# Kernel tuning notes

Measured on AMD Instinct MI355X. Metric: run time of the kernel, lower is better.

Reference implementation:

```python
import jax, jax.numpy as jnp
import numpy as np

N = 100000   # nodes
E = 3200000  # edges (avg degree 32)
K = 3        # num_stacks
L = 4        # num_layers (ARMA iterations)
H = 16       # hidden channels
C = 1        # num_classes
BN_EPS = 1e-5


def setup_inputs() -> dict:
    key = jax.random.key(0)
    ks = jax.random.split(key, 16)
    s = 0.1  # weight scale
    return {
        "x": jax.random.normal(ks[0], (N, 1), dtype=jnp.float32),
        "edge_index": jax.random.randint(ks[1], (2, E), 0, N, dtype=jnp.int64),
        "edge_attr": jax.random.uniform(ks[2], (E,), dtype=jnp.float32),
        "batch": jnp.zeros((N,), dtype=jnp.int64),
        # ARMAConv 1: 1 -> 16, shared weights
        "w1_init": s * jax.random.normal(ks[3], (K, 1, H), dtype=jnp.float32),
        "w1": s * jax.random.normal(ks[4], (K, H, H), dtype=jnp.float32),
        "w1_root": s * jax.random.normal(ks[5], (K, 1, H), dtype=jnp.float32),
        "b1": s * jax.random.normal(ks[6], (K, 1, H), dtype=jnp.float32),
        "bn1_g": jnp.ones((H,), dtype=jnp.float32),
        "bn1_b": jnp.zeros((H,), dtype=jnp.float32),
        # ARMAConv 2: 16 -> 1, shared weights, act=None
        "w2_init": s * jax.random.normal(ks[7], (K, H, C), dtype=jnp.float32),
        "w2": s * jax.random.normal(ks[8], (K, C, C), dtype=jnp.float32),
        "w2_root": s * jax.random.normal(ks[9], (K, H, C), dtype=jnp.float32),
        "b2": s * jax.random.normal(ks[10], (K, 1, C), dtype=jnp.float32),
    }


def _arma_conv(x, row, col, norm, w_init, w, w_root, b, n_layers, use_relu):
    """PyG ARMAConv with shared_weights=True, eval-mode dropout (identity).
    x: [N,Fin]; returns mean over K stacks: [N,Fout]."""
    n = x.shape[0]
    root = jnp.einsum('nf,kfo->kno', x, w_root)      # [K,N,Fout]
    out = jnp.einsum('nf,kfo->kno', x, w_init)       # [K,N,Fout]
    for t in range(n_layers):
        if t > 0:
            out = jnp.einsum('kno,kop->knp', out, w)
        # message: gather at source, scale by norm; aggregate (scatter-add) at target
        m = (out[:, row, :] * norm[None, :, None]).transpose(1, 0, 2)  # [E,K,F]
        out = jax.ops.segment_sum(m, col, num_segments=n).transpose(1, 0, 2)
        out = out + root + b
        if use_relu:
            out = jax.nn.relu(out)
    return out.mean(axis=0)


def reference(x, edge_index, edge_attr, batch, w1_init, w1, w1_root, b1,
              bn1_g, bn1_b, w2_init, w2, w2_root, b2):
    row, col = edge_index[0], edge_index[1]
    n = x.shape[0]
    # gcn_norm without self-loops: D^{-1/2} A D^{-1/2}
    deg = jax.ops.segment_sum(edge_attr, col, num_segments=n)
    dinv = jnp.where(deg > 0, jax.lax.rsqrt(jnp.maximum(deg, 1e-12)), 0.0)
    norm = dinv[row] * edge_attr * dinv[col]

    h = _arma_conv(x, row, col, norm, w1_init, w1, w1_root, b1, L, True)
    # BatchNorm1d (batch statistics) + ReLU; dropout is identity in eval
    mu = h.mean(axis=0)
    var = h.var(axis=0)
    h = (h - mu) * jax.lax.rsqrt(var + BN_EPS) * bn1_g + bn1_b
    h = jax.nn.relu(h)

    h = _arma_conv(h, row, col, norm, w2_init, w2, w2_root, b2, L, False)
    return jax.nn.sigmoid(h)
```

## Files before the change

### kernel.cpp

```cpp
#include <hip/hip_runtime.h>
#include <math.h>

#define N_NODES 100000
#define N_EDGES 3200000
#define KH 48
#define FDIM 64
#define NH 16
#define BN_EPS 1e-5f
#define NBUCK 196
#define BSHIFT 9
#define BMASK 511
#define EPB 16384
#define NBLK1 196
#define CAP 18432
#define FIX 16777216.0f

typedef unsigned long long u64;
typedef unsigned int u32;
typedef unsigned short u16;

__device__ __forceinline__ u16 f2bf(float f) {
  u32 b = __float_as_uint(f);
  b += 0x7FFFu + ((b >> 16) & 1u);
  return (u16)(b >> 16);
}
__device__ __forceinline__ float bf2f(u32 s) {
  return __uint_as_float(s << 16);
}
__device__ __forceinline__ u32 rfl(u32 v) {
  return (u32)__builtin_amdgcn_readfirstlane((int)v);
}

__global__ __launch_bounds__(1024) void bucket_scatter_kernel(
    const int* __restrict__ row, const int* __restrict__ col,
    const float* __restrict__ ea, u32* __restrict__ gcur,
    int2* __restrict__ bucketed) {
  __shared__ u32 bins[NBUCK];
  __shared__ u32 base[NBUCK];
  __shared__ u16 rnk[EPB];
  for (int t = threadIdx.x; t < NBUCK; t += 1024) bins[t] = 0;
  __syncthreads();
  int eb = blockIdx.x * EPB;
  for (int it = 0; it < EPB / 1024; ++it) {
    int i = it * 1024 + threadIdx.x;
    int e = eb + i;
    if (e < N_EDGES) rnk[i] = (u16)atomicAdd(&bins[col[e] >> BSHIFT], 1u);
  }
  __syncthreads();
  for (int t = threadIdx.x; t < NBUCK; t += 1024) {
    u32 c = bins[t];
    if (c) base[t] = (u32)t * CAP + atomicAdd(&gcur[t * 8], c);
  }
  __syncthreads();
  for (int it = 0; it < EPB / 1024; ++it) {
    int i = it * 1024 + threadIdx.x;
    int e = eb + i;
    if (e < N_EDGES) {
      int c = col[e];
      int bkt = c >> BSHIFT, cl = c & BMASK;
      u32 pos = base[bkt] + (u32)rnk[i];
      bucketed[pos] = make_int2((cl << 17) | row[e], __float_as_int(ea[e]));
    }
  }
}

__global__ __launch_bounds__(1024) void node_offs_kernel(
    const int2* __restrict__ bucketed, const u32* __restrict__ gcur,
    const float* __restrict__ x,
    int* __restrict__ offs, float* __restrict__ dinv, u16* __restrict__ zx) {
  __shared__ u32 cnt[512];
  __shared__ u32 degf[512];
  __shared__ u32 red[256];
  __shared__ u32 shmeta[2];
  int t = threadIdx.x;
  int b = blockIdx.x;
  if (t < 512) { cnt[t] = 0; degf[t] = 0; }
  if (t < 256) red[t] = (t < b) ? gcur[t * 8] : 0;
  __syncthreads();
  for (int d = 128; d; d >>= 1) {
    if (t < d) red[t] += red[t + d];
    __syncthreads();
  }
  if (t == 0) { shmeta[0] = red[0]; shmeta[1] = gcur[b * 8]; }
  __syncthreads();
  u32 bst = shmeta[0], fill = shmeta[1];
  u32 s_pad = (u32)b * CAP;
  for (u32 i = t; i < fill; i += 1024) {
    int2 v = bucketed[s_pad + i];
    int cl = (v.x >> 17) & BMASK;
    atomicAdd(&cnt[cl], 1u);
    atomicAdd(&degf[cl], (u32)(__int_as_float(v.y) * FIX));
  }
  __syncthreads();
  u32 v0 = (t < 512) ? cnt[t] : 0;
  for (int d = 1; d < 512; d <<= 1) {
    u32 u = (t < 512 && t >= d) ? cnt[t - d] : 0;
    __syncthreads();
    if (t < 512) cnt[t] += u;
    __syncthreads();
  }
  int n = b * 512 + t;
  if (t < 512 && n < N_NODES) {
    offs[n] = (int)(bst + cnt[t] - v0);
    float dg = (float)degf[t] * (1.0f / FIX);
    float dv = dg > 0.f ? rsqrtf(fmaxf(dg, 1e-12f)) : 0.f;
    dinv[n] = dv;
    zx[n] = f2bf(x[n] * dv);
  }
  if (b == 0 && t == 0) offs[N_NODES] = N_EDGES;
}

__global__ __launch_bounds__(1024) void csr_fill_kernel(
    const int2* __restrict__ bucketed, const u32* __restrict__ gcur,
    const int* __restrict__ offs, u32* __restrict__ csr) {
  __shared__ u32 cur[512];
  __shared__ u32 shfill;
  int t = threadIdx.x;
  int b = blockIdx.x;
  int n = b * 512 + t;
  if (t < 512) cur[t] = (n < N_NODES) ? (u32)offs[n] : 0;
  if (t == 0) shfill = gcur[b * 8];
  __syncthreads();
  u32 fill = shfill;
  u32 s_pad = (u32)b * CAP;
  for (u32 i = t; i < fill; i += 1024) {
    int2 v = bucketed[s_pad + i];
    int cl = (v.x >> 17) & BMASK;
    u32 r = (u32)(v.x & 0x1FFFF);
    u16 w = f2bf(__int_as_float(v.y));
    u32 pos = atomicAdd(&cur[cl], 1u);
    csr[pos] = (r << 15) | (u32)w;
  }
}

__global__ __launch_bounds__(256) void sprop_mid_kernel(
    const u32* __restrict__ csr, const int* __restrict__ offs,
    const u16* __restrict__ zx, const float* __restrict__ dinv,
    const float* __restrict__ x,
    const float* __restrict__ w1i, const float* __restrict__ w1r,
    const float* __restrict__ b1, const float* __restrict__ w1,
    u16* __restrict__ tout) {
  int t = blockIdx.x * 256 + threadIdx.x;
  int n = t >> 4, c = t & 15;
  float a = 0.f;
  int s = offs[n], e = offs[n + 1];
  for (int i = s + c; i < e; i += 16) {
    u32 ee = csr[i];
    a += bf2f(ee & 0x7FFFu) * bf2f((u32)zx[ee >> 15]);
  }
#pragma unroll
  for (int o = 8; o; o >>= 1) a += __shfl_xor(a, o, 64);
  float dn = dinv[n];
  float sn = a * dn;
  float xn = x[n];
  int base = (threadIdx.x & 63) & 48;
#pragma unroll
  for (int k = 0; k < 3; ++k) {
    float u = fmaxf(sn * w1i[k * 16 + c] + xn * w1r[k * 16 + c] + b1[k * 16 + c], 0.f);
    float tf = 0.f;
#pragma unroll
    for (int f = 0; f < 16; ++f) tf += __shfl(u, base + f, 64) * w1[k * 256 + f * 16 + c];
    tout[(size_t)n * FDIM + k * 16 + c] = f2bf(tf * dn);
  }
}

__global__ __launch_bounds__(256) void conv1_prop_kernel(
    const u16* __restrict__ tin, u16* __restrict__ tout, float* __restrict__ hbuf,
    const u32* __restrict__ csr, const int* __restrict__ offs,
    const float* __restrict__ dinv, const float* __restrict__ x,
    const float* __restrict__ w1r, const float* __restrict__ b1,
    const float* __restrict__ w1, int do_t) {
  int lane = threadIdx.x & 63;
  int wid = (blockIdx.x * blockDim.x + threadIdx.x) >> 6;
  int nw = (gridDim.x * blockDim.x) >> 6;
  int c = lane;
  bool act = c < KH;
  float rb = act ? w1r[c] : 0.f;
  float bb = act ? b1[c] : 0.f;
  float wreg[16];
  if (do_t) {
    int k = c >> 4, o = c & 15;
    if (act) {
#pragma unroll
      for (int f = 0; f < 16; ++f) wreg[f] = w1[k * 256 + f * 16 + o];
    } else {
#pragma unroll
      for (int f = 0; f < 16; ++f) wreg[f] = 0.f;
    }
  }
  for (int n = wid; n < N_NODES; n += nw) {
    int nu = __builtin_amdgcn_readfirstlane(n);
    int s = __builtin_amdgcn_readfirstlane(offs[nu]);
    int e = __builtin_amdgcn_readfirstlane(offs[nu + 1]);
    float acc = 0.f;
    int i = s;
    for (; i + 16 <= e; i += 16) {
      u32 e0 = rfl(csr[i]);
      u32 e1 = rfl(csr[i + 1]);
      u32 e2 = rfl(csr[i + 2]);
      u32 e3 = rfl(csr[i + 3]);
      u32 e4 = rfl(csr[i + 4]);
      u32 e5 = rfl(csr[i + 5]);
      u32 e6 = rfl(csr[i + 6]);
      u32 e7 = rfl(csr[i + 7]);
      u32 e8 = rfl(csr[i + 8]);
      u32 e9 = rfl(csr[i + 9]);
      u32 ea0 = rfl(csr[i + 10]);
      u32 eb0 = rfl(csr[i + 11]);
      u32 ec0 = rfl(csr[i + 12]);
      u32 ed0 = rfl(csr[i + 13]);
      u32 ee0 = rfl(csr[i + 14]);
      u32 ef0 = rfl(csr[i + 15]);
      float v0 = bf2f((u32)tin[(e0 >> 15) * FDIM + c]);
      float v1 = bf2f((u32)tin[(e1 >> 15) * FDIM + c]);
      float v2 = bf2f((u32)tin[(e2 >> 15) * FDIM + c]);
      float v3 = bf2f((u32)tin[(e3 >> 15) * FDIM + c]);
      float v4 = bf2f((u32)tin[(e4 >> 15) * FDIM + c]);
      float v5 = bf2f((u32)tin[(e5 >> 15) * FDIM + c]);
      float v6 = bf2f((u32)tin[(e6 >> 15) * FDIM + c]);
      float v7 = bf2f((u32)tin[(e7 >> 15) * FDIM + c]);
      float v8 = bf2f((u32)tin[(e8 >> 15) * FDIM + c]);
      float v9 = bf2f((u32)tin[(e9 >> 15) * FDIM + c]);
      float va = bf2f((u32)tin[(ea0 >> 15) * FDIM + c]);
      float vb = bf2f((u32)tin[(eb0 >> 15) * FDIM + c]);
      float vc = bf2f((u32)tin[(ec0 >> 15) * FDIM + c]);
      float vd = bf2f((u32)tin[(ed0 >> 15) * FDIM + c]);
      float ve = bf2f((u32)tin[(ee0 >> 15) * FDIM + c]);
      float vf = bf2f((u32)tin[(ef0 >> 15) * FDIM + c]);
      acc += bf2f(e0 & 0x7FFFu) * v0 + bf2f(e1 & 0x7FFFu) * v1 +
             bf2f(e2 & 0x7FFFu) * v2 + bf2f(e3 & 0x7FFFu) * v3 +
             bf2f(e4 & 0x7FFFu) * v4 + bf2f(e5 & 0x7FFFu) * v5 +
             bf2f(e6 & 0x7FFFu) * v6 + bf2f(e7 & 0x7FFFu) * v7 +
             bf2f(e8 & 0x7FFFu) * v8 + bf2f(e9 & 0x7FFFu) * v9 +
             bf2f(ea0 & 0x7FFFu) * va + bf2f(eb0 & 0x7FFFu) * vb +
             bf2f(ec0 & 0x7FFFu) * vc + bf2f(ed0 & 0x7FFFu) * vd +
             bf2f(ee0 & 0x7FFFu) * ve + bf2f(ef0 & 0x7FFFu) * vf;
    }
    for (; i + 4 <= e; i += 4) {
      u32 e0 = rfl(csr[i]);
      u32 e1 = rfl(csr[i + 1]);
      u32 e2 = rfl(csr[i + 2]);
      u32 e3 = rfl(csr[i + 3]);
      float v0 = bf2f((u32)tin[(e0 >> 15) * FDIM + c]);
      float v1 = bf2f((u32)tin[(e1 >> 15) * FDIM + c]);
      float v2 = bf2f((u32)tin[(e2 >> 15) * FDIM + c]);
      float v3 = bf2f((u32)tin[(e3 >> 15) * FDIM + c]);
      acc += bf2f(e0 & 0x7FFFu) * v0 + bf2f(e1 & 0x7FFFu) * v1 +
             bf2f(e2 & 0x7FFFu) * v2 + bf2f(e3 & 0x7FFFu) * v3;
    }
    for (; i < e; ++i) {
      u32 ee = rfl(csr[i]);
      acc += bf2f(ee & 0x7FFFu) * bf2f((u32)tin[(ee >> 15) * FDIM + c]);
    }
    float dn = dinv[nu];
    float u = fmaxf(acc * dn + x[nu] * rb + bb, 0.f);
    if (do_t) {
      float tf = 0.f;
      int base = c & 48;
#pragma unroll
      for (int f = 0; f < 16; ++f) tf += __shfl(u, base + f, 64) * wreg[f];
      if (act) tout[(size_t)nu * FDIM + c] = f2bf(tf * dn);
    } else {
      float m1v = __shfl(u, lane + 16, 64);
      float m2v = __shfl(u, lane + 32, 64);
      if (lane < NH) hbuf[(size_t)nu * NH + lane] = (u + m1v + m2v) * (1.f / 3.f);
    }
  }
}

__global__ __launch_bounds__(256) void bn_stats_kernel(
    const float* __restrict__ h, double* __restrict__ stats) {
  __shared__ float ssum[NH], ssq[NH];
  int tid = threadIdx.x;
  if (tid < NH) { ssum[tid] = 0.f; ssq[tid] = 0.f; }
  __syncthreads();
  int n = blockIdx.x * blockDim.x + tid;
  bool valid = n < N_NODES;
  const float4* p = (const float4*)(h + (size_t)(valid ? n : 0) * NH);
  float hv[NH];
#pragma unroll
  for (int q = 0; q < 4; ++q) {
    float4 v = valid ? p[q] : make_float4(0.f, 0.f, 0.f, 0.f);
    hv[q * 4 + 0] = v.x; hv[q * 4 + 1] = v.y; hv[q * 4 + 2] = v.z; hv[q * 4 + 3] = v.w;
  }
#pragma unroll
  for (int f = 0; f < NH; ++f) {
    float s = hv[f], q = hv[f] * hv[f];
    for (int o = 32; o; o >>= 1) { s += __shfl_xor(s, o, 64); q += __shfl_xor(q, o, 64); }
    if ((tid & 63) == 0) { atomicAdd(&ssum[f], s); atomicAdd(&ssq[f], q); }
  }
  __syncthreads();
  if (tid < NH) {
    atomicAdd(&stats[tid], (double)ssum[tid]);
    atomicAdd(&stats[NH + tid], (double)ssq[tid]);
  }
}

__global__ __launch_bounds__(64) void bn_final_kernel(
    const double* __restrict__ stats, const float* __restrict__ g,
    const float* __restrict__ b, float* __restrict__ sc, float* __restrict__ sh) {
  int f = threadIdx.x;
  if (f < NH) {
    double mu = stats[f] / (double)N_NODES;
    double var = stats[NH + f] / (double)N_NODES - mu * mu;
    float scale = g[f] * (float)(1.0 / sqrt(var + (double)BN_EPS));
    sc[f] = scale;
    sh[f] = b[f] - (float)mu * scale;
  }
}

__global__ __launch_bounds__(256) void conv2_init_kernel(
    const float* __restrict__ h, const float* __restrict__ sc, const float* __restrict__ sh,
    const float* __restrict__ dinv,
    const float* __restrict__ w2i, const float* __restrict__ w2r, const float* __restrict__ b2,
    float* __restrict__ P, float* __restrict__ R) {
  int n = blockIdx.x * blockDim.x + threadIdx.x;
  if (n >= N_NODES) return;
  float u[NH];
#pragma unroll
  for (int f = 0; f < NH; ++f) u[f] = fmaxf(h[(size_t)n * NH + f] * sc[f] + sh[f], 0.f);
  float dn = dinv[n];
#pragma unroll
  for (int k = 0; k < 3; ++k) {
    float r = b2[k], o = 0.f;
#pragma unroll
    for (int f = 0; f < NH; ++f) {
      r += u[f] * w2r[k * NH + f];
      o += u[f] * w2i[k * NH + f];
    }
    R[n * 4 + k] = r;
    P[n * 4 + k] = o * dn;
  }
  R[n * 4 + 3] = 0.f;
  P[n * 4 + 3] = 0.f;
}

__global__ __launch_bounds__(256) void conv2_prop_kernel(
    const float* __restrict__ in4, float* __restrict__ out4, float* __restrict__ y,
    const u32* __restrict__ csr, const int* __restrict__ offs,
    const float* __restrict__ dinv,
    const float* __restrict__ R, const float* __restrict__ w2,
    int scale_w2, int final_out) {
  int t = blockIdx.x * 256 + threadIdx.x;
  int n = t >> 4, sub = t & 15;
  float m0 = 1.f, m1 = 1.f, m2 = 1.f;
  if (scale_w2) { m0 = w2[0]; m1 = w2[1]; m2 = w2[2]; }
  int s = offs[n], e = offs[n + 1];
  float a0 = 0.f, a1 = 0.f, a2 = 0.f;
  for (int i = s + sub; i < e; i += 16) {
    u32 ee = csr[i];
    float w = bf2f(ee & 0x7FFFu);
    const float4 v = *(const float4*)(in4 + (size_t)(ee >> 15) * 4);
    a0 += w * v.x;
    a1 += w * v.y;
    a2 += w * v.z;
  }
#pragma unroll
  for (int o = 8; o; o >>= 1) {
    a0 += __shfl_xor(a0, o, 64);
    a1 += __shfl_xor(a1, o, 64);
    a2 += __shfl_xor(a2, o, 64);
  }
  if (sub == 0) {
    float dn = dinv[n];
    a0 = a0 * dn * m0 + R[n * 4 + 0];
    a1 = a1 * dn * m1 + R[n * 4 + 1];
    a2 = a2 * dn * m2 + R[n * 4 + 2];
    if (final_out) {
      float sm = (a0 + a1 + a2) * (1.f / 3.f);
      y[n] = 1.f / (1.f + expf(-sm));
    } else {
      out4[n * 4 + 0] = a0 * dn;
      out4[n * 4 + 1] = a1 * dn;
      out4[n * 4 + 2] = a2 * dn;
      out4[n * 4 + 3] = 0.f;
    }
  }
}

extern "C" void kernel_launch(void* const* d_in, const int* in_sizes, int n_in,
                              void* d_out, int out_size, void* d_ws, size_t ws_size,
                              hipStream_t stream) {
  const float* x   = (const float*)d_in[0];
  const int*   ei  = (const int*)d_in[1];
  const float* ea  = (const float*)d_in[2];
  const float* w1i = (const float*)d_in[4];
  const float* w1  = (const float*)d_in[5];
  const float* w1r = (const float*)d_in[6];
  const float* b1  = (const float*)d_in[7];
  const float* bng = (const float*)d_in[8];
  const float* bnb = (const float*)d_in[9];
  const float* w2i = (const float*)d_in[10];
  const float* w2  = (const float*)d_in[11];
  const float* w2r = (const float*)d_in[12];
  const float* b2  = (const float*)d_in[13];
  float* y = (float*)d_out;

  const int* row = ei;
  const int* col = ei + N_EDGES;

  char* ws = (char*)d_ws;
  size_t off = 0;
  auto alloc = [&](size_t bytes) -> char* {
    char* p = ws + off;
    off += (bytes + 255) & ~(size_t)255;
    return p;
  };
  u32*    gcur   = (u32*)alloc((size_t)NBUCK * 8 * 4);
  int*    offs   = (int*)alloc((size_t)(N_NODES + 1) * 4);
  float*  dinv   = (float*)alloc((size_t)N_NODES * 4);
  u16*    zx     = (u16*)alloc((size_t)N_NODES * 2);
  double* stats  = (double*)alloc(32 * 8);
  float*  bnsc   = (float*)alloc(16 * 4);
  float*  bnsh   = (float*)alloc(16 * 4);
  int2*   bucketed = (int2*)alloc((size_t)NBUCK * CAP * 8);
  u32*    csr    = (u32*)alloc((size_t)N_EDGES * 4);
  u16*    tA     = (u16*)alloc((size_t)N_NODES * FDIM * 2);
  u16*    tB     = (u16*)alloc((size_t)N_NODES * FDIM * 2);
  float*  hbuf   = (float*)alloc((size_t)N_NODES * NH * 4);
  float*  P2     = (float*)alloc((size_t)N_NODES * 4 * 4);
  float*  Q2     = (float*)alloc((size_t)N_NODES * 4 * 4);
  float*  R2     = (float*)alloc((size_t)N_NODES * 4 * 4);
  (void)ws_size; (void)in_sizes; (void)n_in; (void)out_size;

  hipMemsetAsync(gcur, 0, (size_t)NBUCK * 8 * 4, stream);
  hipMemsetAsync(stats, 0, 32 * 8, stream);

  bucket_scatter_kernel<<<NBLK1, 1024, 0, stream>>>(row, col, ea, gcur, bucketed);
  node_offs_kernel<<<NBUCK, 1024, 0, stream>>>(bucketed, gcur, x, offs, dinv, zx);
  csr_fill_kernel<<<NBUCK, 1024, 0, stream>>>(bucketed, gcur, offs, csr);

  const int NPB = 6250;
  sprop_mid_kernel<<<NPB, 256, 0, stream>>>(csr, offs, zx, dinv, x, w1i, w1r, b1, w1, tA);
  conv1_prop_kernel<<<6250, 256, 0, stream>>>(tA, tB, nullptr, csr, offs, dinv, x, w1r, b1, w1, 1);
  conv1_prop_kernel<<<6250, 256, 0, stream>>>(tB, tA, nullptr, csr, offs, dinv, x, w1r, b1, w1, 1);
  conv1_prop_kernel<<<6250, 256, 0, stream>>>(tA, nullptr, hbuf, csr, offs, dinv, x, w1r, b1, w1, 0);

  bn_stats_kernel<<<(N_NODES + 255) / 256, 256, 0, stream>>>(hbuf, stats);
  bn_final_kernel<<<1, 64, 0, stream>>>(stats, bng, bnb, bnsc, bnsh);
  conv2_init_kernel<<<(N_NODES + 255) / 256, 256, 0, stream>>>(
      hbuf, bnsc, bnsh, dinv, w2i, w2r, b2, P2, R2);

  conv2_prop_kernel<<<NPB, 256, 0, stream>>>(P2, Q2, nullptr, csr, offs, dinv, R2, w2, 0, 0);
  conv2_prop_kernel<<<NPB, 256, 0, stream>>>(Q2, P2, nullptr, csr, offs, dinv, R2, w2, 1, 0);
  conv2_prop_kernel<<<NPB, 256, 0, stream>>>(P2, Q2, nullptr, csr, offs, dinv, R2, w2, 1, 0);
  conv2_prop_kernel<<<NPB, 256, 0, stream>>>(Q2, P2, y, csr, offs, dinv, R2, w2, 1, 1);
}
```

Baseline: 478.9 us.

## Fuse CSR fill into node offsets kernel and software-pipeline edge index loads

Merges the csr_fill kernel into node_offs so each bucket's cursor is initialised in shared memory and the bucketed edges are scattered right after the prefix scan. This drops one launch and the global offs re-read. Separately, conv1_prop now double-buffers the 16-edge CSR index loads, prefetching the next block while gathering the current one, to hide index-load latency. The cost is higher register pressure from holding 32 scalar indices.

```diff
diff --git a/kernel.cpp b/kernel.cpp
--- a/kernel.cpp
+++ b/kernel.cpp
@@ -64,12 +64,14 @@
   }
 }
 
-__global__ __launch_bounds__(1024) void node_offs_kernel(
+__global__ __launch_bounds__(1024) void node_offs_csr_kernel(
     const int2* __restrict__ bucketed, const u32* __restrict__ gcur,
     const float* __restrict__ x,
-    int* __restrict__ offs, float* __restrict__ dinv, u16* __restrict__ zx) {
+    int* __restrict__ offs, float* __restrict__ dinv, u16* __restrict__ zx,
+    u32* __restrict__ csr) {
   __shared__ u32 cnt[512];
   __shared__ u32 degf[512];
+  __shared__ u32 cur[512];
   __shared__ u32 red[256];
   __shared__ u32 shmeta[2];
   int t = threadIdx.x;
@@ -100,29 +102,21 @@
     __syncthreads();
   }
   int n = b * 512 + t;
-  if (t < 512 && n < N_NODES) {
-    offs[n] = (int)(bst + cnt[t] - v0);
-    float dg = (float)degf[t] * (1.0f / FIX);
-    float dv = dg > 0.f ? rsqrtf(fmaxf(dg, 1e-12f)) : 0.f;
-    dinv[n] = dv;
-    zx[n] = f2bf(x[n] * dv);
+  if (t < 512) {
+    if (n < N_NODES) {
+      u32 off0 = bst + cnt[t] - v0;
+      offs[n] = (int)off0;
+      cur[t] = off0;
+      float dg = (float)degf[t] * (1.0f / FIX);
+      float dv = dg > 0.f ? rsqrtf(fmaxf(dg, 1e-12f)) : 0.f;
+      dinv[n] = dv;
+      zx[n] = f2bf(x[n] * dv);
+    } else {
+      cur[t] = 0;
+    }
   }
   if (b == 0 && t == 0) offs[N_NODES] = N_EDGES;
-}
-
-__global__ __launch_bounds__(1024) void csr_fill_kernel(
-    const int2* __restrict__ bucketed, const u32* __restrict__ gcur,
-    const int* __restrict__ offs, u32* __restrict__ csr) {
-  __shared__ u32 cur[512];
-  __shared__ u32 shfill;
-  int t = threadIdx.x;
-  int b = blockIdx.x;
-  int n = b * 512 + t;
-  if (t < 512) cur[t] = (n < N_NODES) ? (u32)offs[n] : 0;
-  if (t == 0) shfill = gcur[b * 8];
-  __syncthreads();
-  u32 fill = shfill;
-  u32 s_pad = (u32)b * CAP;
+  __syncthreads();
   for (u32 i = t; i < fill; i += 1024) {
     int2 v = bucketed[s_pad + i];
     int cl = (v.x >> 17) & BMASK;
@@ -163,6 +157,49 @@
     tout[(size_t)n * FDIM + k * 16 + c] = f2bf(tf * dn);
   }
 }
+
+#define DECL16(p) u32 p##0, p##1, p##2, p##3, p##4, p##5, p##6, p##7, \
+                      p##8, p##9, p##10, p##11, p##12, p##13, p##14, p##15
+#define LOAD16(p, base) \
+  p##0 = rfl(csr[(base)]);      p##1 = rfl(csr[(base) + 1]);  \
+  p##2 = rfl(csr[(base) + 2]);  p##3 = rfl(csr[(base) + 3]);  \
+  p##4 = rfl(csr[(base) + 4]);  p##5 = rfl(csr[(base) + 5]);  \
+  p##6 = rfl(csr[(base) + 6]);  p##7 = rfl(csr[(base) + 7]);  \
+  p##8 = rfl(csr[(base) + 8]);  p##9 = rfl(csr[(base) + 9]);  \
+  p##10 = rfl(csr[(base) + 10]); p##11 = rfl(csr[(base) + 11]); \
+  p##12 = rfl(csr[(base) + 12]); p##13 = rfl(csr[(base) + 13]); \
+  p##14 = rfl(csr[(base) + 14]); p##15 = rfl(csr[(base) + 15])
+#define COPY16(d, s2) \
+  d##0 = s2##0; d##1 = s2##1; d##2 = s2##2; d##3 = s2##3; \
+  d##4 = s2##4; d##5 = s2##5; d##6 = s2##6; d##7 = s2##7; \
+  d##8 = s2##8; d##9 = s2##9; d##10 = s2##10; d##11 = s2##11; \
+  d##12 = s2##12; d##13 = s2##13; d##14 = s2##14; d##15 = s2##15
+#define PROC16(p) do { \
+  float v0 = bf2f((u32)tin[(p##0 >> 15) * FDIM + c]); \
+  float v1 = bf2f((u32)tin[(p##1 >> 15) * FDIM + c]); \
+  float v2 = bf2f((u32)tin[(p##2 >> 15) * FDIM + c]); \
+  float v3 = bf2f((u32)tin[(p##3 >> 15) * FDIM + c]); \
+  float v4 = bf2f((u32)tin[(p##4 >> 15) * FDIM + c]); \
+  float v5 = bf2f((u32)tin[(p##5 >> 15) * FDIM + c]); \
+  float v6 = bf2f((u32)tin[(p##6 >> 15) * FDIM + c]); \
+  float v7 = bf2f((u32)tin[(p##7 >> 15) * FDIM + c]); \
+  float v8 = bf2f((u32)tin[(p##8 >> 15) * FDIM + c]); \
+  float v9 = bf2f((u32)tin[(p##9 >> 15) * FDIM + c]); \
+  float va = bf2f((u32)tin[(p##10 >> 15) * FDIM + c]); \
+  float vb = bf2f((u32)tin[(p##11 >> 15) * FDIM + c]); \
+  float vc = bf2f((u32)tin[(p##12 >> 15) * FDIM + c]); \
+  float vd = bf2f((u32)tin[(p##13 >> 15) * FDIM + c]); \
+  float ve = bf2f((u32)tin[(p##14 >> 15) * FDIM + c]); \
+  float vf = bf2f((u32)tin[(p##15 >> 15) * FDIM + c]); \
+  acc += bf2f(p##0 & 0x7FFFu) * v0 + bf2f(p##1 & 0x7FFFu) * v1 + \
+         bf2f(p##2 & 0x7FFFu) * v2 + bf2f(p##3 & 0x7FFFu) * v3 + \
+         bf2f(p##4 & 0x7FFFu) * v4 + bf2f(p##5 & 0x7FFFu) * v5 + \
+         bf2f(p##6 & 0x7FFFu) * v6 + bf2f(p##7 & 0x7FFFu) * v7 + \
+         bf2f(p##8 & 0x7FFFu) * v8 + bf2f(p##9 & 0x7FFFu) * v9 + \
+         bf2f(p##10 & 0x7FFFu) * va + bf2f(p##11 & 0x7FFFu) * vb + \
+         bf2f(p##12 & 0x7FFFu) * vc + bf2f(p##13 & 0x7FFFu) * vd + \
+         bf2f(p##14 & 0x7FFFu) * ve + bf2f(p##15 & 0x7FFFu) * vf; \
+} while (0)
 
 __global__ __launch_bounds__(256) void conv1_prop_kernel(
     const u16* __restrict__ tin, u16* __restrict__ tout, float* __restrict__ hbuf,
@@ -194,47 +231,20 @@
     int e = __builtin_amdgcn_readfirstlane(offs[nu + 1]);
     float acc = 0.f;
     int i = s;
-    for (; i + 16 <= e; i += 16) {
-      u32 e0 = rfl(csr[i]);
-      u32 e1 = rfl(csr[i + 1]);
-      u32 e2 = rfl(csr[i + 2]);
-      u32 e3 = rfl(csr[i + 3]);
-      u32 e4 = rfl(csr[i + 4]);
-      u32 e5 = rfl(csr[i + 5]);
-      u32 e6 = rfl(csr[i + 6]);
-      u32 e7 = rfl(csr[i + 7]);
-      u32 e8 = rfl(csr[i + 8]);
-      u32 e9 = rfl(csr[i + 9]);
-      u32 ea0 = rfl(csr[i + 10]);
-      u32 eb0 = rfl(csr[i + 11]);
-      u32 ec0 = rfl(csr[i + 12]);
-      u32 ed0 = rfl(csr[i + 13]);
-      u32 ee0 = rfl(csr[i + 14]);
-      u32 ef0 = rfl(csr[i + 15]);
-      float v0 = bf2f((u32)tin[(e0 >> 15) * FDIM + c]);
-      float v1 = bf2f((u32)tin[(e1 >> 15) * FDIM + c]);
-      float v2 = bf2f((u32)tin[(e2 >> 15) * FDIM + c]);
-      float v3 = bf2f((u32)tin[(e3 >> 15) * FDIM + c]);
-      float v4 = bf2f((u32)tin[(e4 >> 15) * FDIM + c]);
-      float v5 = bf2f((u32)tin[(e5 >> 15) * FDIM + c]);
-      float v6 = bf2f((u32)tin[(e6 >> 15) * FDIM + c]);
-      float v7 = bf2f((u32)tin[(e7 >> 15) * FDIM + c]);
-      float v8 = bf2f((u32)tin[(e8 >> 15) * FDIM + c]);
-      float v9 = bf2f((u32)tin[(e9 >> 15) * FDIM + c]);
-      float va = bf2f((u32)tin[(ea0 >> 15) * FDIM + c]);
-      float vb = bf2f((u32)tin[(eb0 >> 15) * FDIM + c]);
-      float vc = bf2f((u32)tin[(ec0 >> 15) * FDIM + c]);
-      float vd = bf2f((u32)tin[(ed0 >> 15) * FDIM + c]);
-      float ve = bf2f((u32)tin[(ee0 >> 15) * FDIM + c]);
-      float vf = bf2f((u32)tin[(ef0 >> 15) * FDIM + c]);
-      acc += bf2f(e0 & 0x7FFFu) * v0 + bf2f(e1 & 0x7FFFu) * v1 +
-             bf2f(e2 & 0x7FFFu) * v2 + bf2f(e3 & 0x7FFFu) * v3 +
-             bf2f(e4 & 0x7FFFu) * v4 + bf2f(e5 & 0x7FFFu) * v5 +
-             bf2f(e6 & 0x7FFFu) * v6 + bf2f(e7 & 0x7FFFu) * v7 +
-             bf2f(e8 & 0x7FFFu) * v8 + bf2f(e9 & 0x7FFFu) * v9 +
-             bf2f(ea0 & 0x7FFFu) * va + bf2f(eb0 & 0x7FFFu) * vb +
-             bf2f(ec0 & 0x7FFFu) * vc + bf2f(ed0 & 0x7FFFu) * vd +
-             bf2f(ee0 & 0x7FFFu) * ve + bf2f(ef0 & 0x7FFFu) * vf;
+    int nblk = (e - s) >> 4;
+    if (nblk > 0) {
+      DECL16(a);
+      DECL16(b);
+      LOAD16(a, i);
+      for (int blk = 1; blk < nblk; ++blk) {
+        int j = i + 16;
+        LOAD16(b, j);
+        PROC16(a);
+        COPY16(a, b);
+        i = j;
+      }
+      PROC16(a);
+      i += 16;
     }
     for (; i + 4 <= e; i += 4) {
       u32 e0 = rfl(csr[i]);
@@ -427,8 +437,7 @@
   hipMemsetAsync(stats, 0, 32 * 8, stream);
 
   bucket_scatter_kernel<<<NBLK1, 1024, 0, stream>>>(row, col, ea, gcur, bucketed);
-  node_offs_kernel<<<NBUCK, 1024, 0, stream>>>(bucketed, gcur, x, offs, dinv, zx);
-  csr_fill_kernel<<<NBUCK, 1024, 0, stream>>>(bucketed, gcur, offs, csr);
+  node_offs_csr_kernel<<<NBUCK, 1024, 0, stream>>>(bucketed, gcur, x, offs, dinv, zx, csr);
 
   const int NPB = 6250;
   sprop_mid_kernel<<<NPB, 256, 0, stream>>>(csr, offs, zx, dinv, x, w1i, w1r, b1, w1, tA);
```

Result: no change. 469.6 us (-1.9%).
